# Optimization experiments

Measured on AMD Instinct MI355X. Metric: run time of the kernel, lower is better.

## Reference

```python
import jax, jax.numpy as jnp
import numpy as np

NQ = 6; DM = 128; CH = 4; SEQ = 2048; CHUNK = 16; BATCH = 128
NFP = 5 * NQ * 2   # feature params for 2 layers
NMP = 5 * NQ * 2   # mixing params for 2 layers

# ---- batched gate matrices (theta: (B,)) ----

def _rx(t):
    c = jnp.cos(t / 2).astype(jnp.complex64)
    s = (-1j * jnp.sin(t / 2)).astype(jnp.complex64)
    return jnp.stack([jnp.stack([c, s], -1), jnp.stack([s, c], -1)], -2)

def _ry(t):
    c = jnp.cos(t / 2).astype(jnp.complex64)
    s = jnp.sin(t / 2).astype(jnp.complex64)
    return jnp.stack([jnp.stack([c, -s], -1), jnp.stack([s, c], -1)], -2)

def _rz(t):
    e = jnp.exp(-1j * t.astype(jnp.complex64) / 2)
    z = jnp.zeros_like(e)
    return jnp.stack([jnp.stack([e, z], -1), jnp.stack([z, jnp.conj(e)], -1)], -2)

def _crx(t):
    B = t.shape[0]
    r = _rx(t)
    I = jnp.broadcast_to(jnp.eye(2, dtype=jnp.complex64), (B, 2, 2))
    Z = jnp.zeros((B, 2, 2), jnp.complex64)
    return jnp.concatenate([jnp.concatenate([I, Z], -1), jnp.concatenate([Z, r], -1)], -2)

# ---- batched statevector gate application; state: (B, 2, ..., 2) with axis 1+w = wire w ----

def _ap1(s, U, w):
    s = jnp.moveaxis(s, 1 + w, 1)
    sh = s.shape
    s = jnp.einsum('bij,bjr->bir', U, s.reshape(sh[0], 2, -1)).reshape(sh)
    return jnp.moveaxis(s, 1, 1 + w)

def _ap2(s, U, w0, w1):
    s = jnp.moveaxis(s, (1 + w0, 1 + w1), (1, 2))
    sh = s.shape
    s = jnp.einsum('bij,bjr->bir', U, s.reshape(sh[0], 4, -1)).reshape(sh)
    return jnp.moveaxis(s, (1, 2), (1 + w0, 1 + w1))

def _ansatz(s, p, off):
    # RX,RY,RZ on each qubit, then forward CRX ring, then backward CRX ring
    for i in range(NQ):
        s = _ap1(s, _rx(p[:, off + 3 * i]), i)
        s = _ap1(s, _ry(p[:, off + 3 * i + 1]), i)
        s = _ap1(s, _rz(p[:, off + 3 * i + 2]), i)
    off += 3 * NQ
    for i in range(NQ):
        s = _ap2(s, _crx(p[:, off]), i, (i + 1) % NQ)
        off += 1
    for i in range(NQ - 1, -1, -1):
        s = _ap2(s, _crx(p[:, off]), i, (i - 1) % NQ)
        off += 1
    return s, off

def _circuit(angles, fp, mp):
    B = angles.shape[0]
    s = jnp.zeros((B, 2 ** NQ), jnp.complex64).at[:, 0].set(1.0).reshape((B,) + (2,) * NQ)
    for i in range(NQ):                      # RY input embedding
        s = _ap1(s, _ry(angles[:, i]), i)
    off = 0
    for _ in range(2):                        # feature layers
        s, off = _ansatz(s, fp, off)
    off = 0
    for _ in range(2):                        # mixing layers
        s, off = _ansatz(s, mp, off)
    xs, ys, zs = [], [], []
    for i in range(NQ):                       # <X_i>, <Y_i>, <Z_i>
        v = jnp.moveaxis(s, 1 + i, 1).reshape(B, 2, -1)
        a, b = v[:, 0], v[:, 1]
        ab = jnp.sum(jnp.conj(a) * b, -1)
        xs.append(2 * jnp.real(ab))
        ys.append(2 * jnp.imag(ab))
        zs.append(jnp.sum(jnp.abs(a) ** 2 - jnp.abs(b) ** 2, -1))
    return jnp.stack(xs + ys + zs, 1)         # (B, 18) ordered X..Y..Z

def _ln(x, g, b, eps=1e-5):
    m = x.mean(-1, keepdims=True)
    v = ((x - m) ** 2).mean(-1, keepdims=True)
    return (x - m) / jnp.sqrt(v + eps) * g + b

def _fwd(x, conv_w, conv_b, ln1_g, ln1_b, ca1_w, ca1_b, ca2_w, ca2_b, pp_w, pp_b,
         ep_w, ep_b, op_w, op_b, ln2_g, ln2_b, sa1_w, sa1_b, sa2_w, sa2_b,
         cl1_w, cl1_b, cl2_w, cl2_b):
    B, C, S = x.shape
    h = jax.lax.conv_general_dilated(x, conv_w, (1,), [(1, 1)],
                                     dimension_numbers=('NCH', 'OIH', 'NCH')) + conv_b[None, :, None]
    h = jnp.transpose(h, (0, 2, 1))           # (B, S, D)
    h = _ln(h, ln1_g, ln1_b)
    nchunks = S // CHUNK
    h = h.reshape(B * nchunks, CHUNK, DM)
    sc = jnp.tanh(h @ ca1_w + ca1_b) @ ca2_w + ca2_b
    w = jax.nn.softmax(sc, axis=1)
    summ = jnp.sum(w * h, axis=1)             # (B*nchunks, D)
    ap = summ @ pp_w + pp_b
    fp, mp = ap[:, :NFP], ap[:, NFP:]
    ang = jnp.tanh(summ @ ep_w + ep_b) * np.pi
    q = _circuit(ang, fp, mp)                 # (B*nchunks, 18)
    cf = jax.nn.silu(_ln(q @ op_w + op_b, ln2_g, ln2_b))  # dropout = eval identity
    cf = cf.reshape(B, nchunks, DM)
    ss = jnp.tanh(cf @ sa1_w + sa1_b) @ sa2_w + sa2_b
    sw = jax.nn.softmax(ss, axis=1)
    rep = jnp.sum(sw * cf, axis=1)
    return jax.nn.silu(rep @ cl1_w + cl1_b) @ cl2_w + cl2_b

def setup_inputs() -> dict:
    key = jax.random.key(0)
    ks = jax.random.split(key, 16)
    n = lambda k, sh: (jax.random.normal(k, sh, jnp.float32) * 0.05)
    return {
        'x': jax.random.normal(ks[0], (BATCH, CH, SEQ), jnp.float32),
        'conv_w': n(ks[1], (DM, CH, 3)), 'conv_b': jnp.zeros((DM,), jnp.float32),
        'ln1_g': jnp.ones((DM,), jnp.float32), 'ln1_b': jnp.zeros((DM,), jnp.float32),
        'ca1_w': n(ks[2], (DM, DM // 4)), 'ca1_b': jnp.zeros((DM // 4,), jnp.float32),
        'ca2_w': n(ks[3], (DM // 4, 1)), 'ca2_b': jnp.zeros((1,), jnp.float32),
        'pp_w': n(ks[4], (DM, NFP + NMP)), 'pp_b': jnp.zeros((NFP + NMP,), jnp.float32),
        'ep_w': n(ks[5], (DM, NQ)), 'ep_b': jnp.zeros((NQ,), jnp.float32),
        'op_w': n(ks[6], (3 * NQ, DM)), 'op_b': jnp.zeros((DM,), jnp.float32),
        'ln2_g': jnp.ones((DM,), jnp.float32), 'ln2_b': jnp.zeros((DM,), jnp.float32),
        'sa1_w': n(ks[7], (DM, DM // 4)), 'sa1_b': jnp.zeros((DM // 4,), jnp.float32),
        'sa2_w': n(ks[8], (DM // 4, 1)), 'sa2_b': jnp.zeros((1,), jnp.float32),
        'cl1_w': n(ks[9], (DM, DM // 2)), 'cl1_b': jnp.zeros((DM // 2,), jnp.float32),
        'cl2_w': n(ks[10], (DM // 2, 2)), 'cl2_b': jnp.zeros((2,), jnp.float32),
    }

def reference(x, conv_w, conv_b, ln1_g, ln1_b, ca1_w, ca1_b, ca2_w, ca2_b, pp_w, pp_b,
              ep_w, ep_b, op_w, op_b, ln2_g, ln2_b, sa1_w, sa1_b, sa2_w, sa2_b,
              cl1_w, cl1_b, cl2_w, cl2_b):
    return _fwd(x, conv_w, conv_b, ln1_g, ln1_b, ca1_w, ca1_b, ca2_w, ca2_b, pp_w, pp_b,
                ep_w, ep_b, op_w, op_b, ln2_g, ln2_b, sa1_w, sa1_b, sa2_w, sa2_b,
                cl1_w, cl1_b, cl2_w, cl2_b)
```

## Files before the change

kernel.cpp:

```cpp
#include <hip/hip_runtime.h>
#include <math.h>


constexpr int kNQ    = 6;
constexpr int kDM    = 128;
constexpr int kCH    = 4;
constexpr int kSEQ   = 2048;
constexpr int kCHUNK = 16;
constexpr int kBATCH = 128;
constexpr int kNCH   = kSEQ / kCHUNK;
constexpr int kNP    = 120;
constexpr float kPI  = 3.14159265358979323846f;

typedef __attribute__((ext_vector_type(8))) short bf16x8;
typedef __attribute__((ext_vector_type(4))) float f32x4;

__device__ __forceinline__ float fast_tanh(float x) {
  float e = __expf(-2.f * fabsf(x));
  float r = (1.f - e) * __builtin_amdgcn_rcpf(1.f + e);
  return copysignf(r, x);
}
__device__ __forceinline__ float fast_silu(float x) {
  return x * __builtin_amdgcn_rcpf(1.f + __expf(-x));
}

template <int XM>
__device__ __forceinline__ float qp(float v) {
  constexpr int ctrl = (XM == 1) ? 0xB1 : 0x4E;
  return __int_as_float(
      __builtin_amdgcn_update_dpp(0, __float_as_int(v), ctrl, 0xF, 0xF, true));
}


template <int RB>
__device__ __forceinline__ void rx_reg(float c, float s, float* sr, float* si) {
#pragma unroll
  for (int r0 = 0; r0 < 16; ++r0) {
    if (r0 & RB) continue;
    int r1 = r0 | RB;
    float ar = sr[r0], ai = si[r0], br = sr[r1], bi = si[r1];
    sr[r0] = fmaf(c, ar,  s * bi);  si[r0] = fmaf(c, ai, -s * br);
    sr[r1] = fmaf(c, br,  s * ai);  si[r1] = fmaf(c, bi, -s * ar);
  }
}

template <int RB>
__device__ __forceinline__ void ry_reg(float c, float s, float* sr, float* si) {
#pragma unroll
  for (int r0 = 0; r0 < 16; ++r0) {
    if (r0 & RB) continue;
    int r1 = r0 | RB;
    float ar = sr[r0], ai = si[r0], br = sr[r1], bi = si[r1];
    sr[r0] = fmaf(c, ar, -s * br);  si[r0] = fmaf(c, ai, -s * bi);
    sr[r1] = fmaf(s, ar,  c * br);  si[r1] = fmaf(s, ai,  c * bi);
  }
}

template <int RB>
__device__ __forceinline__ void rz_reg(float c, float s, float* sr, float* si) {
#pragma unroll
  for (int r = 0; r < 16; ++r) {
    float sp = (r & RB) ? s : -s;
    float ar = sr[r], ai = si[r];
    sr[r] = fmaf(c, ar, -sp * ai);
    si[r] = fmaf(c, ai,  sp * ar);
  }
}

template <int XM>
__device__ __forceinline__ void rx_lane(float c, float s, float* sr, float* si) {
#pragma unroll
  for (int r = 0; r < 16; ++r) {
    float pr = qp<XM>(sr[r]), pi = qp<XM>(si[r]);
    sr[r] = fmaf(c, sr[r],  s * pi);
    si[r] = fmaf(c, si[r], -s * pr);
  }
}

template <int XM>
__device__ __forceinline__ void ry_lane(float c, float sg, float* sr, float* si) {
#pragma unroll
  for (int r = 0; r < 16; ++r) {
    float pr = qp<XM>(sr[r]), pi = qp<XM>(si[r]);
    sr[r] = fmaf(c, sr[r], sg * pr);
    si[r] = fmaf(c, si[r], sg * pi);
  }
}

__device__ __forceinline__ void rz_lane(float c, float sp, float* sr, float* si) {
#pragma unroll
  for (int r = 0; r < 16; ++r) {
    float ar = sr[r], ai = si[r];
    sr[r] = fmaf(c, ar, -sp * ai);
    si[r] = fmaf(c, ai,  sp * ar);
  }
}

template <int RB, int CB>
__device__ __forceinline__ void crx_reg_reg(float c, float s, float* sr, float* si) {
#pragma unroll
  for (int r0 = 0; r0 < 16; ++r0) {
    if ((r0 & RB) || !(r0 & CB)) continue;
    int r1 = r0 | RB;
    float ar = sr[r0], ai = si[r0], br = sr[r1], bi = si[r1];
    sr[r0] = fmaf(c, ar,  s * bi);  si[r0] = fmaf(c, ai, -s * br);
    sr[r1] = fmaf(c, br,  s * ai);  si[r1] = fmaf(c, bi, -s * ar);
  }
}

template <int XM, int CB>
__device__ __forceinline__ void crx_reg_lane(float c, float s, float* sr, float* si) {
#pragma unroll
  for (int r = 0; r < 16; ++r) {
    if (!(r & CB)) continue;
    float pr = qp<XM>(sr[r]), pi = qp<XM>(si[r]);
    sr[r] = fmaf(c, sr[r],  s * pi);
    si[r] = fmaf(c, si[r], -s * pr);
  }
}

template <int RB>
__device__ __forceinline__ void meas_reg(const float* sr, const float* si,
                                         float& tr, float& ti, float& zz) {
  tr = 0.f; ti = 0.f; zz = 0.f;
#pragma unroll
  for (int r0 = 0; r0 < 16; ++r0) {
    float n = fmaf(sr[r0], sr[r0], si[r0] * si[r0]);
    zz += (r0 & RB) ? -n : n;
    if (r0 & RB) continue;
    int r1 = r0 | RB;
    tr = fmaf(sr[r0], sr[r1], fmaf(si[r0], si[r1], tr));
    ti = fmaf(sr[r0], si[r1], fmaf(-si[r0], sr[r1], ti));
  }
  tr += qp<1>(tr); tr += qp<2>(tr);
  ti += qp<1>(ti); ti += qp<2>(ti);
  zz += qp<1>(zz); zz += qp<2>(zz);
}


__device__ __forceinline__ void circ_from_cs(const float2* __restrict__ cp,
                                             int l, int b0, int b1,
                                             float* __restrict__ res) {
  float sr[16], si[16];
#pragma unroll
  for (int r = 0; r < 16; ++r) { sr[r] = 0.f; si[r] = 0.f; }
  sr[0] = (l == 0) ? 1.f : 0.f;

  {
    float2 q0 = cp[0], q1 = cp[1], q2 = cp[2], q3 = cp[3], q4 = cp[4], q5 = cp[5];
    ry_lane<2>(q0.x, b0 ? q0.y : -q0.y, sr, si);
    ry_lane<1>(q1.x, b1 ? q1.y : -q1.y, sr, si);
    ry_reg<8>(q2.x, q2.y, sr, si);
    ry_reg<4>(q3.x, q3.y, sr, si);
    ry_reg<2>(q4.x, q4.y, sr, si);
    ry_reg<1>(q5.x, q5.y, sr, si);
  }

  for (int a = 0; a < 4; ++a) {
    const float2* pb = cp + 6 + a * 30;
    float2 t;
    t = pb[0];  rx_lane<2>(t.x, t.y, sr, si);
    t = pb[1];  ry_lane<2>(t.x, b0 ? t.y : -t.y, sr, si);
    t = pb[2];  rz_lane   (t.x, b0 ? t.y : -t.y, sr, si);
    t = pb[3];  rx_lane<1>(t.x, t.y, sr, si);
    t = pb[4];  ry_lane<1>(t.x, b1 ? t.y : -t.y, sr, si);
    t = pb[5];  rz_lane   (t.x, b1 ? t.y : -t.y, sr, si);
    t = pb[6];  rx_reg<8>(t.x, t.y, sr, si);
    t = pb[7];  ry_reg<8>(t.x, t.y, sr, si);
    t = pb[8];  rz_reg<8>(t.x, t.y, sr, si);
    t = pb[9];  rx_reg<4>(t.x, t.y, sr, si);
    t = pb[10]; ry_reg<4>(t.x, t.y, sr, si);
    t = pb[11]; rz_reg<4>(t.x, t.y, sr, si);
    t = pb[12]; rx_reg<2>(t.x, t.y, sr, si);
    t = pb[13]; ry_reg<2>(t.x, t.y, sr, si);
    t = pb[14]; rz_reg<2>(t.x, t.y, sr, si);
    t = pb[15]; rx_reg<1>(t.x, t.y, sr, si);
    t = pb[16]; ry_reg<1>(t.x, t.y, sr, si);
    t = pb[17]; rz_reg<1>(t.x, t.y, sr, si);
    t = pb[18]; { float c2 = b0 ? t.x : 1.f, s2 = b0 ? t.y : 0.f; rx_lane<1>(c2, s2, sr, si); }
    t = pb[19]; { float c2 = b1 ? t.x : 1.f, s2 = b1 ? t.y : 0.f; rx_reg<8>(c2, s2, sr, si); }
    t = pb[20]; crx_reg_reg<4, 8>(t.x, t.y, sr, si);
    t = pb[21]; crx_reg_reg<2, 4>(t.x, t.y, sr, si);
    t = pb[22]; crx_reg_reg<1, 2>(t.x, t.y, sr, si);
    t = pb[23]; crx_reg_lane<2, 1>(t.x, t.y, sr, si);
    t = pb[24]; crx_reg_reg<2, 1>(t.x, t.y, sr, si);
    t = pb[25]; crx_reg_reg<4, 2>(t.x, t.y, sr, si);
    t = pb[26]; crx_reg_reg<8, 4>(t.x, t.y, sr, si);
    t = pb[27]; crx_reg_lane<1, 8>(t.x, t.y, sr, si);
    t = pb[28]; { float c2 = b1 ? t.x : 1.f, s2 = b1 ? t.y : 0.f; rx_lane<2>(c2, s2, sr, si); }
    t = pb[29]; { float c2 = b0 ? t.x : 1.f, s2 = b0 ? t.y : 0.f; rx_reg<1>(c2, s2, sr, si); }
  }

  {
    float tr = 0.f, ti = 0.f, zz = 0.f;
#pragma unroll
    for (int r = 0; r < 16; ++r) {
      float pr = qp<2>(sr[r]), pi = qp<2>(si[r]);
      tr = fmaf(sr[r], pr, fmaf(si[r], pi, tr));
      ti = fmaf(sr[r], pi, fmaf(-si[r], pr, ti));
      zz = fmaf(sr[r], sr[r], fmaf(si[r], si[r], zz));
    }
    tr = b0 ? 0.f : tr;  ti = b0 ? 0.f : ti;  zz = b0 ? -zz : zz;
    tr += qp<1>(tr); tr += qp<2>(tr);
    ti += qp<1>(ti); ti += qp<2>(ti);
    zz += qp<1>(zz); zz += qp<2>(zz);
    res[0] = 2.f * tr; res[6] = 2.f * ti; res[12] = zz;
  }
  {
    float tr = 0.f, ti = 0.f, zz = 0.f;
#pragma unroll
    for (int r = 0; r < 16; ++r) {
      float pr = qp<1>(sr[r]), pi = qp<1>(si[r]);
      tr = fmaf(sr[r], pr, fmaf(si[r], pi, tr));
      ti = fmaf(sr[r], pi, fmaf(-si[r], pr, ti));
      zz = fmaf(sr[r], sr[r], fmaf(si[r], si[r], zz));
    }
    tr = b1 ? 0.f : tr;  ti = b1 ? 0.f : ti;  zz = b1 ? -zz : zz;
    tr += qp<1>(tr); tr += qp<2>(tr);
    ti += qp<1>(ti); ti += qp<2>(ti);
    zz += qp<1>(zz); zz += qp<2>(zz);
    res[1] = 2.f * tr; res[7] = 2.f * ti; res[13] = zz;
  }
  {
    float tr, ti, zz;
    meas_reg<8>(sr, si, tr, ti, zz); res[2] = 2.f*tr; res[8]  = 2.f*ti; res[14] = zz;
    meas_reg<4>(sr, si, tr, ti, zz); res[3] = 2.f*tr; res[9]  = 2.f*ti; res[15] = zz;
    meas_reg<2>(sr, si, tr, ti, zz); res[4] = 2.f*tr; res[10] = 2.f*ti; res[16] = zz;
    meas_reg<1>(sr, si, tr, ti, zz); res[5] = 2.f*tr; res[11] = 2.f*ti; res[17] = zz;
  }
}


__global__ __launch_bounds__(128) void k_pre8(
    const float* __restrict__ x,
    const float* __restrict__ conv_w, const float* __restrict__ conv_b,
    const float* __restrict__ ln1_g,  const float* __restrict__ ln1_b,
    const float* __restrict__ ca1_w,  const float* __restrict__ ca1_b,
    const float* __restrict__ ca2_w,  const float* __restrict__ ca2_b,
    const float* __restrict__ pp_w,   const float* __restrict__ pp_b,
    const float* __restrict__ ep_w,   const float* __restrict__ ep_b,
    float* __restrict__ outb, int emit_cs)
{
  constexpr int NC = 8;

  __shared__ __align__(16) float xs[kCH][NC * kCHUNK + 4];
  __shared__ __align__(16) float hbuf[kCHUNK][132];
  __shared__ __align__(16) float spart[2][16];
  __shared__ __align__(16) float wl[kCHUNK];
  __shared__ __align__(16) float sums[NC][kDM];
  __shared__ float mrow[kCHUNK], irow[kCHUNK];

  const int tid    = threadIdx.x;
  const int chunk0 = blockIdx.x * NC;
  const int b      = chunk0 >> 7;
  const int tloc   = (chunk0 & 127) * kCHUNK;
  const int d      = tid;
  const int lane   = tid & 63;
  const int wv     = tid >> 6;
  const int col    = (lane & 15) + 16 * wv;
  const int qd     = lane >> 4;

  float w12[12];
  {
    const float4* cw = (const float4*)(conv_w + d * 12);
    float4 a0 = cw[0], a1 = cw[1], a2 = cw[2];
    w12[0]=a0.x; w12[1]=a0.y; w12[2]=a0.z; w12[3]=a0.w;
    w12[4]=a1.x; w12[5]=a1.y; w12[6]=a1.z; w12[7]=a1.w;
    w12[8]=a2.x; w12[9]=a2.y; w12[10]=a2.z; w12[11]=a2.w;
  }
  float cb = conv_b[d];
  float g1 = ln1_g[d], b1 = ln1_b[d];
  float cb1 = ca1_b[col], cw2 = ca2_w[col], cb2 = ca2_b[0];

  bf16x8 bhi[4], blo[4];
#pragma unroll
  for (int ks = 0; ks < 4; ++ks)
#pragma unroll
    for (int jj = 0; jj < 8; ++jj) {
      float bvf = ca1_w[(ks * 32 + qd * 8 + jj) * 32 + col];
      unsigned bb = __float_as_uint(bvf);
      bhi[ks][jj] = (short)(bb >> 16);
      float lf = bvf - __uint_as_float(bb & 0xffff0000u);
      blo[ks][jj] = (short)(__float_as_uint(lf) >> 16);
    }

#pragma unroll
  for (int ch = 0; ch < kCH; ++ch) {
#pragma unroll
    for (int base = 0; base < 2; ++base) {
      int pos = base * 128 + tid;
      if (pos < NC * kCHUNK + 2) {
        int s = tloc - 1 + pos;
        float v = 0.f;
        if (s >= 0 && s < kSEQ) v = x[((size_t)b * kCH + ch) * kSEQ + s];
        xs[ch][pos] = v;
      }
    }
  }
  __syncthreads();

  for (int c = 0; c < NC; ++c) {
    float h[kCHUNK];
#pragma unroll
    for (int t = 0; t < kCHUNK; ++t) h[t] = cb;
#pragma unroll
    for (int ch = 0; ch < kCH; ++ch) {
      const float4* xp = (const float4*)&xs[ch][c * kCHUNK];
      float4 v0 = xp[0], v1 = xp[1], v2 = xp[2], v3 = xp[3], v4 = xp[4];
      float xr[18];
      xr[0]=v0.x; xr[1]=v0.y; xr[2]=v0.z; xr[3]=v0.w;
      xr[4]=v1.x; xr[5]=v1.y; xr[6]=v1.z; xr[7]=v1.w;
      xr[8]=v2.x; xr[9]=v2.y; xr[10]=v2.z; xr[11]=v2.w;
      xr[12]=v3.x; xr[13]=v3.y; xr[14]=v3.z; xr[15]=v3.w;
      xr[16]=v4.x; xr[17]=v4.y;
      float c0 = w12[ch*3+0], c1 = w12[ch*3+1], c2 = w12[ch*3+2];
#pragma unroll
      for (int t = 0; t < kCHUNK; ++t)
        h[t] = fmaf(xr[t], c0, fmaf(xr[t+1], c1, fmaf(xr[t+2], c2, h[t])));
    }
#pragma unroll
    for (int t = 0; t < kCHUNK; ++t) hbuf[t][d] = h[t];
    __syncthreads();

    {
      int row = tid >> 3, k = tid & 7;
      const float4* rp = (const float4*)&hbuf[row][k * 16];
      float s1 = 0.f, s2 = 0.f;
#pragma unroll
      for (int q = 0; q < 4; ++q) {
        float4 v = rp[q];
        s1 += v.x + v.y + v.z + v.w;
        s2 = fmaf(v.x,v.x,s2); s2 = fmaf(v.y,v.y,s2);
        s2 = fmaf(v.z,v.z,s2); s2 = fmaf(v.w,v.w,s2);
      }
#pragma unroll
      for (int o = 1; o < 8; o <<= 1) {
        s1 += __shfl_xor(s1, o, 64);
        s2 += __shfl_xor(s2, o, 64);
      }
      if (k == 0) {
        float m = s1 * (1.f / kDM);
        mrow[row] = m;
        irow[row] = rsqrtf(s2 * (1.f / kDM) - m * m + 1e-5f);
      }
    }
    __syncthreads();

#pragma unroll
    for (int t = 0; t < kCHUNK; ++t) {
      h[t] = fmaf((h[t] - mrow[t]) * irow[t], g1, b1);
      unsigned hb = __float_as_uint(h[t]);
      float lof = h[t] - __uint_as_float(hb & 0xffff0000u);
      unsigned pk = (hb >> 16) | (__float_as_uint(lof) & 0xffff0000u);
      ((unsigned*)&hbuf[t][0])[d] = pk;
    }
    __syncthreads();

    f32x4 acc = {0.f, 0.f, 0.f, 0.f};
    {
      const unsigned* hrow = (const unsigned*)&hbuf[lane & 15][0];
#pragma unroll
      for (int ks = 0; ks < 4; ++ks) {
        const uint4* ap = (const uint4*)(hrow + ks * 32 + qd * 8);
        uint4 w0 = ap[0], w1 = ap[1];
        bf16x8 ahi, alo;
        ahi[0] = (short)(w0.x & 0xffff); ahi[1] = (short)(w0.y & 0xffff);
        ahi[2] = (short)(w0.z & 0xffff); ahi[3] = (short)(w0.w & 0xffff);
        ahi[4] = (short)(w1.x & 0xffff); ahi[5] = (short)(w1.y & 0xffff);
        ahi[6] = (short)(w1.z & 0xffff); ahi[7] = (short)(w1.w & 0xffff);
        alo[0] = (short)(w0.x >> 16); alo[1] = (short)(w0.y >> 16);
        alo[2] = (short)(w0.z >> 16); alo[3] = (short)(w0.w >> 16);
        alo[4] = (short)(w1.x >> 16); alo[5] = (short)(w1.y >> 16);
        alo[6] = (short)(w1.z >> 16); alo[7] = (short)(w1.w >> 16);
        acc = __builtin_amdgcn_mfma_f32_16x16x32_bf16(ahi, bhi[ks], acc, 0, 0, 0);
        acc = __builtin_amdgcn_mfma_f32_16x16x32_bf16(ahi, blo[ks], acc, 0, 0, 0);
        acc = __builtin_amdgcn_mfma_f32_16x16x32_bf16(alo, bhi[ks], acc, 0, 0, 0);
      }
    }

    {
      float ev[4];
#pragma unroll
      for (int r = 0; r < 4; ++r)
        ev[r] = fast_tanh(acc[r] + cb1) * cw2;
#pragma unroll
      for (int o = 1; o < 16; o <<= 1)
#pragma unroll
        for (int r = 0; r < 4; ++r) ev[r] += __shfl_xor(ev[r], o, 64);
      if ((lane & 15) == 0)
        *(float4*)&spart[wv][qd * 4] = make_float4(ev[0], ev[1], ev[2], ev[3]);
    }
    __syncthreads();

    if (tid < 16) {
      float scl = spart[0][tid] + spart[1][tid] + cb2;
      float mx = scl;
#pragma unroll
      for (int o = 1; o < 16; o <<= 1) mx = fmaxf(mx, __shfl_xor(mx, o, 64));
      float e = __expf(scl - mx);
      float se = e;
#pragma unroll
      for (int o = 1; o < 16; o <<= 1) se += __shfl_xor(se, o, 64);
      wl[tid] = e * (1.f / se);
    }
    __syncthreads();

    {
      const float4* w4 = (const float4*)wl;
      float4 wa = w4[0], wb = w4[1], wc = w4[2], wd = w4[3];
      float acc2 = 0.f;
      acc2 = fmaf(wa.x, h[0],  acc2); acc2 = fmaf(wa.y, h[1],  acc2);
      acc2 = fmaf(wa.z, h[2],  acc2); acc2 = fmaf(wa.w, h[3],  acc2);
      acc2 = fmaf(wb.x, h[4],  acc2); acc2 = fmaf(wb.y, h[5],  acc2);
      acc2 = fmaf(wb.z, h[6],  acc2); acc2 = fmaf(wb.w, h[7],  acc2);
      acc2 = fmaf(wc.x, h[8],  acc2); acc2 = fmaf(wc.y, h[9],  acc2);
      acc2 = fmaf(wc.z, h[10], acc2); acc2 = fmaf(wc.w, h[11], acc2);
      acc2 = fmaf(wd.x, h[12], acc2); acc2 = fmaf(wd.y, h[13], acc2);
      acc2 = fmaf(wd.z, h[14], acc2); acc2 = fmaf(wd.w, h[15], acc2);
      sums[c][d] = acc2;
    }
  }
  __syncthreads();

  if (tid < kNP + kNQ) {
    const bool isep = (tid >= kNP);
    const int  jj   = tid - kNP;
    const float* wp = isep ? (ep_w + jj) : (pp_w + tid);
    const int  ws   = isep ? kNQ : kNP;
    const int  ws2  = ws * 2, ws3 = ws * 3, ws4 = ws * 4;
    float bias = isep ? ep_b[jj] : pp_b[tid];
    float accp[NC];
#pragma unroll
    for (int c = 0; c < NC; ++c) accp[c] = bias;
#pragma unroll 4
    for (int q4 = 0; q4 < 32; ++q4) {
      float w0 = wp[0], w1 = wp[ws], w2 = wp[ws2], w3 = wp[ws3];
      wp += ws4;
#pragma unroll
      for (int c = 0; c < NC; ++c) {
        float4 s = *(const float4*)&sums[c][q4 * 4];
        accp[c] = fmaf(s.x, w0, fmaf(s.y, w1, fmaf(s.z, w2, fmaf(s.w, w3, accp[c]))));
      }
    }
    const int slot = isep ? jj : (6 + tid);
#pragma unroll
    for (int c = 0; c < NC; ++c) {
      int chunkg = chunk0 + c;
      float ha = isep ? (0.5f * fast_tanh(accp[c]) * kPI) : (0.5f * accp[c]);
      if (emit_cs) {
        ((float2*)(outb + (size_t)chunkg * 256))[slot] =
            make_float2(__cosf(ha), __sinf(ha));
      } else {
        outb[(size_t)chunkg * 126 + slot] = ha;
      }
    }
  }
}


constexpr int kCsStride = 260;

__global__ __launch_bounds__(256) void k_circ_post(
    const float* __restrict__ csA,
    const float* __restrict__ op_w, const float* __restrict__ op_b,
    const float* __restrict__ ln2_g, const float* __restrict__ ln2_b,
    const float* __restrict__ sa1_w, const float* __restrict__ sa1_b,
    const float* __restrict__ sa2_w, const float* __restrict__ sa2_b,
    float* __restrict__ cf, float* __restrict__ sclb)
{
  __shared__ __align__(16) float lds[16 * kCsStride];
  __shared__ __align__(16) float qvs[16][19];
  __shared__ __align__(16) float cfs[2][132];
  __shared__ float part1[2][32];
  __shared__ float redA[2][2], redB[2][2];

  const int tid = threadIdx.x;

  {
    const float4* src = (const float4*)(csA + (size_t)blockIdx.x * 16 * 256);
#pragma unroll
    for (int jq = 0; jq < 4; ++jq) {
      int idx = jq * 256 + tid;
      int ic = idx >> 6, ln = idx & 63;
      *(float4*)&lds[ic * kCsStride + ln * 4] = src[idx];
    }
  }
  __syncthreads();

  if (tid < 64) {
    const int c  = tid >> 2;
    const int l  = tid & 3;
    const int b0 = (l >> 1) & 1;
    const int b1 = l & 1;
    float res[18];
    circ_from_cs((const float2*)&lds[c * kCsStride], l, b0, b1, res);
    if (l == 0) {
#pragma unroll
      for (int k = 0; k < 18; ++k) qvs[c][k] = res[k];
    }
  }

  const int d    = tid & 127;
  const int slot = tid >> 7;
  const int j    = d & 31;
  const int sub  = d >> 5;
  float ow[18];
#pragma unroll
  for (int k = 0; k < 18; ++k) ow[k] = op_w[k * kDM + d];
  float ob = op_b[d], g2 = ln2_g[d], b2 = ln2_b[d];
  float wreg[32];
  {
    const float* wp2 = sa1_w + (sub * 32) * 32 + j;
#pragma unroll
    for (int k = 0; k < 32; ++k) wreg[k] = wp2[k * 32];
  }
  float s1b = sa1_b[j], s2w = sa2_w[j], s2b = sa2_b[0];
  __syncthreads();

  for (int i = 0; i < 8; ++i) {
    const int c      = slot * 8 + i;
    const int chunkg = blockIdx.x * 16 + c;

    float qv[18];
#pragma unroll
    for (int k = 0; k < 18; ++k) qv[k] = qvs[c][k];
    float acc = ob;
#pragma unroll
    for (int k = 0; k < 18; ++k) acc = fmaf(qv[k], ow[k], acc);

    float v = acc, v2 = acc * acc;
#pragma unroll
    for (int o = 32; o; o >>= 1) { v += __shfl_xor(v, o, 64); v2 += __shfl_xor(v2, o, 64); }
    if ((d & 63) == 0) { redA[slot][d >> 6] = v; redB[slot][d >> 6] = v2; }
    __syncthreads();
    float ss1 = redA[slot][0] + redA[slot][1];
    float ss2 = redB[slot][0] + redB[slot][1];
    float m = ss1 * (1.f / kDM);
    float var = ss2 * (1.f / kDM) - m * m;
    float xn = fmaf((acc - m) * rsqrtf(var + 1e-5f), g2, b2);
    float cfv = fast_silu(xn);
    cf[(size_t)chunkg * kDM + d] = cfv;
    cfs[slot][d] = cfv;
    __syncthreads();

    float acc2 = 0.f;
#pragma unroll
    for (int q = 0; q < 8; ++q) {
      float4 hv = *(const float4*)&cfs[slot][sub * 32 + q * 4];
      acc2 = fmaf(hv.x, wreg[q*4+0], acc2);
      acc2 = fmaf(hv.y, wreg[q*4+1], acc2);
      acc2 = fmaf(hv.z, wreg[q*4+2], acc2);
      acc2 = fmaf(hv.w, wreg[q*4+3], acc2);
    }
    acc2 += __shfl_xor(acc2, 32, 64);
    if (sub == 2) part1[slot][j] = acc2;
    __syncthreads();
    if (d < 32) {
      float hv = fast_tanh(acc2 + part1[slot][j] + s1b) * s2w;
#pragma unroll
      for (int o = 16; o; o >>= 1) hv += __shfl_xor(hv, o, 64);
      if (j == 0) sclb[chunkg] = hv + s2b;
    }
  }
}


__global__ __launch_bounds__(64) void k_circ_cs(const float* __restrict__ csA,
                                                float* __restrict__ qv_g)
{
  __shared__ __align__(16) float lds[16 * kCsStride];

  const int lane  = threadIdx.x;
  const int c     = lane >> 2;
  const int l     = lane & 3;
  const int chunk = blockIdx.x * 16 + c;
  const int b0 = (l >> 1) & 1;
  const int b1 = l & 1;

  {
    const float4* src = (const float4*)(csA + (size_t)blockIdx.x * 16 * 256);
#pragma unroll
    for (int i = 0; i < 16; ++i) {
      float4 v = src[i * 64 + lane];
      *(float4*)&lds[i * kCsStride + lane * 4] = v;
    }
  }
  __syncthreads();

  float res[18];
  circ_from_cs((const float2*)&lds[c * kCsStride], l, b0, b1, res);

  if (l == 0) {
    float* qo = qv_g + (size_t)chunk * 18;
#pragma unroll
    for (int k = 0; k < 18; ++k) qo[k] = res[k];
  }
}


__global__ __launch_bounds__(64) void k_circ(const float* __restrict__ csb_g,
                                             float* __restrict__ qv_g)
{
  const int lane  = threadIdx.x;
  const int c     = lane >> 2;
  const int l     = lane & 3;
  const int chunk = blockIdx.x * 16 + c;
  const float* cp = csb_g + (size_t)chunk * 126;
  const int b0 = (l >> 1) & 1;
  const int b1 = l & 1;

  float sr[16], si[16];
#pragma unroll
  for (int r = 0; r < 16; ++r) { sr[r] = 0.f; si[r] = 0.f; }
  sr[0] = (l == 0) ? 1.f : 0.f;

  {
    float gc[6], gs[6];
#pragma unroll
    for (int g = 0; g < 6; ++g) { float th = cp[g]; gc[g] = __cosf(th); gs[g] = __sinf(th); }
    ry_lane<2>(gc[0], b0 ? gs[0] : -gs[0], sr, si);
    ry_lane<1>(gc[1], b1 ? gs[1] : -gs[1], sr, si);
    ry_reg<8>(gc[2], gs[2], sr, si);
    ry_reg<4>(gc[3], gs[3], sr, si);
    ry_reg<2>(gc[4], gs[4], sr, si);
    ry_reg<1>(gc[5], gs[5], sr, si);
  }

  for (int a = 0; a < 4; ++a) {
    const float* pb = cp + 6 + a * 30;
    float gc[30], gs[30];
#pragma unroll
    for (int g = 0; g < 30; ++g) { float th = pb[g]; gc[g] = __cosf(th); gs[g] = __sinf(th); }
    rx_lane<2>(gc[0], gs[0], sr, si);
    ry_lane<2>(gc[1], b0 ? gs[1] : -gs[1], sr, si);
    rz_lane   (gc[2], b0 ? gs[2] : -gs[2], sr, si);
    rx_lane<1>(gc[3], gs[3], sr, si);
    ry_lane<1>(gc[4], b1 ? gs[4] : -gs[4], sr, si);
    rz_lane   (gc[5], b1 ? gs[5] : -gs[5], sr, si);
    rx_reg<8>(gc[6],  gs[6],  sr, si);  ry_reg<8>(gc[7],  gs[7],  sr, si);  rz_reg<8>(gc[8],  gs[8],  sr, si);
    rx_reg<4>(gc[9],  gs[9],  sr, si);  ry_reg<4>(gc[10], gs[10], sr, si);  rz_reg<4>(gc[11], gs[11], sr, si);
    rx_reg<2>(gc[12], gs[12], sr, si);  ry_reg<2>(gc[13], gs[13], sr, si);  rz_reg<2>(gc[14], gs[14], sr, si);
    rx_reg<1>(gc[15], gs[15], sr, si);  ry_reg<1>(gc[16], gs[16], sr, si);  rz_reg<1>(gc[17], gs[17], sr, si);
    { float c2 = b0 ? gc[18] : 1.f, s2 = b0 ? gs[18] : 0.f; rx_lane<1>(c2, s2, sr, si); }
    { float c2 = b1 ? gc[19] : 1.f, s2 = b1 ? gs[19] : 0.f; rx_reg<8>(c2, s2, sr, si); }
    crx_reg_reg<4, 8>(gc[20], gs[20], sr, si);
    crx_reg_reg<2, 4>(gc[21], gs[21], sr, si);
    crx_reg_reg<1, 2>(gc[22], gs[22], sr, si);
    crx_reg_lane<2, 1>(gc[23], gs[23], sr, si);
    crx_reg_reg<2, 1>(gc[24], gs[24], sr, si);
    crx_reg_reg<4, 2>(gc[25], gs[25], sr, si);
    crx_reg_reg<8, 4>(gc[26], gs[26], sr, si);
    crx_reg_lane<1, 8>(gc[27], gs[27], sr, si);
    { float c2 = b1 ? gc[28] : 1.f, s2 = b1 ? gs[28] : 0.f; rx_lane<2>(c2, s2, sr, si); }
    { float c2 = b0 ? gc[29] : 1.f, s2 = b0 ? gs[29] : 0.f; rx_reg<1>(c2, s2, sr, si); }
  }

  float res[18];
  {
    float tr = 0.f, ti = 0.f, zz = 0.f;
#pragma unroll
    for (int r = 0; r < 16; ++r) {
      float pr = qp<2>(sr[r]), pi = qp<2>(si[r]);
      tr = fmaf(sr[r], pr, fmaf(si[r], pi, tr));
      ti = fmaf(sr[r], pi, fmaf(-si[r], pr, ti));
      zz = fmaf(sr[r], sr[r], fmaf(si[r], si[r], zz));
    }
    tr = b0 ? 0.f : tr;  ti = b0 ? 0.f : ti;  zz = b0 ? -zz : zz;
    tr += qp<1>(tr); tr += qp<2>(tr);
    ti += qp<1>(ti); ti += qp<2>(ti);
    zz += qp<1>(zz); zz += qp<2>(zz);
    res[0] = 2.f * tr; res[6] = 2.f * ti; res[12] = zz;
  }
  {
    float tr = 0.f, ti = 0.f, zz = 0.f;
#pragma unroll
    for (int r = 0; r < 16; ++r) {
      float pr = qp<1>(sr[r]), pi = qp<1>(si[r]);
      tr = fmaf(sr[r], pr, fmaf(si[r], pi, tr));
      ti = fmaf(sr[r], pi, fmaf(-si[r], pr, ti));
      zz = fmaf(sr[r], sr[r], fmaf(si[r], si[r], zz));
    }
    tr = b1 ? 0.f : tr;  ti = b1 ? 0.f : ti;  zz = b1 ? -zz : zz;
    tr += qp<1>(tr); tr += qp<2>(tr);
    ti += qp<1>(ti); ti += qp<2>(ti);
    zz += qp<1>(zz); zz += qp<2>(zz);
    res[1] = 2.f * tr; res[7] = 2.f * ti; res[13] = zz;
  }
  {
    float tr, ti, zz;
    meas_reg<8>(sr, si, tr, ti, zz); res[2] = 2.f*tr; res[8]  = 2.f*ti; res[14] = zz;
    meas_reg<4>(sr, si, tr, ti, zz); res[3] = 2.f*tr; res[9]  = 2.f*ti; res[15] = zz;
    meas_reg<2>(sr, si, tr, ti, zz); res[4] = 2.f*tr; res[10] = 2.f*ti; res[16] = zz;
    meas_reg<1>(sr, si, tr, ti, zz); res[5] = 2.f*tr; res[11] = 2.f*ti; res[17] = zz;
  }
  if (l == 0) {
    float* qo = qv_g + (size_t)chunk * 18;
#pragma unroll
    for (int k = 0; k < 18; ++k) qo[k] = res[k];
  }
}


__global__ __launch_bounds__(128) void k_post(
    const float* __restrict__ qv_g,
    const float* __restrict__ op_w, const float* __restrict__ op_b,
    const float* __restrict__ ln2_g, const float* __restrict__ ln2_b,
    const float* __restrict__ sa1_w, const float* __restrict__ sa1_b,
    const float* __restrict__ sa2_w, const float* __restrict__ sa2_b,
    float* __restrict__ cf, float* __restrict__ sclb)
{
  __shared__ float cfs[132];
  __shared__ float part1[32];
  __shared__ float red[4];

  const int chunk = blockIdx.x, tid = threadIdx.x, d = tid;
  const int j = tid & 31, sub = tid >> 5;

  float qv[18];
  {
    const float* qpp = qv_g + (size_t)chunk * 18;
#pragma unroll
    for (int k = 0; k < 18; ++k) qv[k] = qpp[k];
  }
  float acc = op_b[d];
#pragma unroll
  for (int k = 0; k < 18; ++k) acc = fmaf(qv[k], op_w[k * kDM + d], acc);

  float v = acc, v2 = acc * acc;
#pragma unroll
  for (int o = 32; o; o >>= 1) { v += __shfl_xor(v, o, 64); v2 += __shfl_xor(v2, o, 64); }
  if ((tid & 63) == 0) { red[tid >> 6] = v; red[2 + (tid >> 6)] = v2; }
  __syncthreads();
  float s1 = red[0] + red[1], s2 = red[2] + red[3];
  float m = s1 * (1.f / kDM);
  float var = s2 * (1.f / kDM) - m * m;
  float xn = fmaf((acc - m) * rsqrtf(var + 1e-5f), ln2_g[d], ln2_b[d]);
  float cfv = fast_silu(xn);
  cf[(size_t)chunk * kDM + d] = cfv;
  cfs[d] = cfv;
  __syncthreads();

  float acc2 = 0.f;
  {
    const float* wp2 = sa1_w + (sub * 32) * 32 + j;
#pragma unroll
    for (int q = 0; q < 8; ++q) {
      float4 hv = *(const float4*)&cfs[sub * 32 + q * 4];
      acc2 = fmaf(hv.x, wp2[(q*4+0)*32], acc2);
      acc2 = fmaf(hv.y, wp2[(q*4+1)*32], acc2);
      acc2 = fmaf(hv.z, wp2[(q*4+2)*32], acc2);
      acc2 = fmaf(hv.w, wp2[(q*4+3)*32], acc2);
    }
  }
  acc2 += __shfl_xor(acc2, 32, 64);
  if (sub == 2) part1[j] = acc2;
  __syncthreads();
  if (tid < 32) {
    float hv = fast_tanh(acc2 + part1[j] + sa1_b[j]) * sa2_w[j];
#pragma unroll
    for (int o = 16; o; o >>= 1) hv += __shfl_xor(hv, o, 64);
    if (j == 0) sclb[chunk] = hv + sa2_b[0];
  }
}


__global__ __launch_bounds__(512) void k_pool_cf(
    const float* __restrict__ cf, const float* __restrict__ scl,
    const float* __restrict__ cl1_w, const float* __restrict__ cl1_b,
    const float* __restrict__ cl2_w, const float* __restrict__ cl2_b,
    float* __restrict__ out)
{
  __shared__ float wl[kNCH];
  __shared__ float rep4[4][kDM];
  __shared__ float ulp[8][64];
  __shared__ float ul[64];
  __shared__ float red2[16];
  int b = blockIdx.x, tid = threadIdx.x;
  int idx = tid & 127, wid = tid >> 6;
  float s = scl[b*kNCH + idx];
  float mx = s;
#pragma unroll
  for (int o = 32; o; o >>= 1) mx = fmaxf(mx, __shfl_xor(mx,o,64));
  if ((tid & 63) == 0) red2[wid] = mx;
  __syncthreads();
  mx = fmaxf(red2[0], red2[1]);
  float e = __expf(s - mx);
  float se = e;
#pragma unroll
  for (int o = 32; o; o >>= 1) se += __shfl_xor(se,o,64);
  if ((tid & 63) == 0) red2[8+wid] = se;
  if (tid < kNCH) wl[tid] = e;
  __syncthreads();
  float inv = 1.f/(red2[8]+red2[9]);
  {
    int dd = tid & 127, qq = tid >> 7;
    const float* cfb = cf + (size_t)b*kNCH*kDM + (size_t)qq*32*kDM;
    const float* wlq = wl + qq*32;
    float a0=0,a1=0,a2=0,a3=0;
// ... 385 lines not shown
```

Before: 192.0 us.

## Fuse per-qubit RX/RY/RZ rotations into single precomputed 2x2 unitaries

Adds a cooperative pre-pass where all 256 threads compose each qubit's RX·RY·RZ triple (and the input RY embedding for the first layer) into one general 2x2 complex unitary and store it in shared memory. The circuit simulation then applies one generic gate per qubit instead of three or four separate rotations, which cuts per-thread gate work in the serial 64-thread circuit phase. In exchange it adds an extra shared buffer, another barrier, and denser complex arithmetic per gate application.

```diff
diff --git a/kernel.cpp b/kernel.cpp
--- a/kernel.cpp
+++ b/kernel.cpp
@@ -135,6 +135,38 @@
   tr += qp<1>(tr); tr += qp<2>(tr);
   ti += qp<1>(ti); ti += qp<2>(ti);
   zz += qp<1>(zz); zz += qp<2>(zz);
+}
+
+
+template <int RB>
+__device__ __forceinline__ void gen_reg(const float4 u0, const float4 u1,
+                                        float* sr, float* si) {
+#pragma unroll
+  for (int r0 = 0; r0 < 16; ++r0) {
+    if (r0 & RB) continue;
+    int r1 = r0 | RB;
+    float p0r = sr[r0], p0i = si[r0], p1r = sr[r1], p1i = si[r1];
+    sr[r0] = fmaf(u0.x, p0r, fmaf(-u0.y, p0i, fmaf(u0.z, p1r, -u0.w * p1i)));
+    si[r0] = fmaf(u0.x, p0i, fmaf( u0.y, p0r, fmaf(u0.z, p1i,  u0.w * p1r)));
+    sr[r1] = fmaf(u1.x, p0r, fmaf(-u1.y, p0i, fmaf(u1.z, p1r, -u1.w * p1i)));
+    si[r1] = fmaf(u1.x, p0i, fmaf( u1.y, p0r, fmaf(u1.z, p1i,  u1.w * p1r)));
+  }
+}
+
+template <int XM>
+__device__ __forceinline__ void gen_lane(const float4 u0, const float4 u1,
+                                         int bsel, float* sr, float* si) {
+  float m0r = bsel ? u1.z : u0.x;
+  float m0i = bsel ? u1.w : u0.y;
+  float m1r = bsel ? u1.x : u0.z;
+  float m1i = bsel ? u1.y : u0.w;
+#pragma unroll
+  for (int r = 0; r < 16; ++r) {
+    float pr = qp<XM>(sr[r]), pi = qp<XM>(si[r]);
+    float xr = sr[r], xi = si[r];
+    sr[r] = fmaf(m0r, xr, fmaf(-m0i, xi, fmaf(m1r, pr, -m1i * pi)));
+    si[r] = fmaf(m0r, xi, fmaf( m0i, xr, fmaf(m1r, pi,  m1i * pr)));
+  }
 }
 
 
@@ -231,6 +263,80 @@
 }
 
 
+__device__ __forceinline__ void circ_fused(const float2* __restrict__ cp,
+                                           const float* __restrict__ fp,
+                                           int l, int b0, int b1,
+                                           float* __restrict__ res) {
+  float sr[16], si[16];
+#pragma unroll
+  for (int r = 0; r < 16; ++r) { sr[r] = 0.f; si[r] = 0.f; }
+  sr[0] = (l == 0) ? 1.f : 0.f;
+
+  for (int a = 0; a < 4; ++a) {
+    const float4* fg = (const float4*)(fp + a * 48);
+    gen_lane<2>(fg[0],  fg[1],  b0, sr, si);
+    gen_lane<1>(fg[2],  fg[3],  b1, sr, si);
+    gen_reg<8> (fg[4],  fg[5],  sr, si);
+    gen_reg<4> (fg[6],  fg[7],  sr, si);
+    gen_reg<2> (fg[8],  fg[9],  sr, si);
+    gen_reg<1> (fg[10], fg[11], sr, si);
+
+    const float2* pb = cp + 6 + a * 30;
+    float2 t;
+    t = pb[18]; { float c2 = b0 ? t.x : 1.f, s2 = b0 ? t.y : 0.f; rx_lane<1>(c2, s2, sr, si); }
+    t = pb[19]; { float c2 = b1 ? t.x : 1.f, s2 = b1 ? t.y : 0.f; rx_reg<8>(c2, s2, sr, si); }
+    t = pb[20]; crx_reg_reg<4, 8>(t.x, t.y, sr, si);
+    t = pb[21]; crx_reg_reg<2, 4>(t.x, t.y, sr, si);
+    t = pb[22]; crx_reg_reg<1, 2>(t.x, t.y, sr, si);
+    t = pb[23]; crx_reg_lane<2, 1>(t.x, t.y, sr, si);
+    t = pb[24]; crx_reg_reg<2, 1>(t.x, t.y, sr, si);
+    t = pb[25]; crx_reg_reg<4, 2>(t.x, t.y, sr, si);
+    t = pb[26]; crx_reg_reg<8, 4>(t.x, t.y, sr, si);
+    t = pb[27]; crx_reg_lane<1, 8>(t.x, t.y, sr, si);
+    t = pb[28]; { float c2 = b1 ? t.x : 1.f, s2 = b1 ? t.y : 0.f; rx_lane<2>(c2, s2, sr, si); }
+    t = pb[29]; { float c2 = b0 ? t.x : 1.f, s2 = b0 ? t.y : 0.f; rx_reg<1>(c2, s2, sr, si); }
+  }
+
+  {
+    float tr = 0.f, ti = 0.f, zz = 0.f;
+#pragma unroll
+    for (int r = 0; r < 16; ++r) {
+      float pr = qp<2>(sr[r]), pi = qp<2>(si[r]);
+      tr = fmaf(sr[r], pr, fmaf(si[r], pi, tr));
+      ti = fmaf(sr[r], pi, fmaf(-si[r], pr, ti));
+      zz = fmaf(sr[r], sr[r], fmaf(si[r], si[r], zz));
+    }
+    tr = b0 ? 0.f : tr;  ti = b0 ? 0.f : ti;  zz = b0 ? -zz : zz;
+    tr += qp<1>(tr); tr += qp<2>(tr);
+    ti += qp<1>(ti); ti += qp<2>(ti);
+    zz += qp<1>(zz); zz += qp<2>(zz);
+    res[0] = 2.f * tr; res[6] = 2.f * ti; res[12] = zz;
+  }
+  {
+    float tr = 0.f, ti = 0.f, zz = 0.f;
+#pragma unroll
+    for (int r = 0; r < 16; ++r) {
+      float pr = qp<1>(sr[r]), pi = qp<1>(si[r]);
+      tr = fmaf(sr[r], pr, fmaf(si[r], pi, tr));
+      ti = fmaf(sr[r], pi, fmaf(-si[r], pr, ti));
+      zz = fmaf(sr[r], sr[r], fmaf(si[r], si[r], zz));
+    }
+    tr = b1 ? 0.f : tr;  ti = b1 ? 0.f : ti;  zz = b1 ? -zz : zz;
+    tr += qp<1>(tr); tr += qp<2>(tr);
+    ti += qp<1>(ti); ti += qp<2>(ti);
+    zz += qp<1>(zz); zz += qp<2>(zz);
+    res[1] = 2.f * tr; res[7] = 2.f * ti; res[13] = zz;
+  }
+  {
+    float tr, ti, zz;
+    meas_reg<8>(sr, si, tr, ti, zz); res[2] = 2.f*tr; res[8]  = 2.f*ti; res[14] = zz;
+    meas_reg<4>(sr, si, tr, ti, zz); res[3] = 2.f*tr; res[9]  = 2.f*ti; res[15] = zz;
+    meas_reg<2>(sr, si, tr, ti, zz); res[4] = 2.f*tr; res[10] = 2.f*ti; res[16] = zz;
+    meas_reg<1>(sr, si, tr, ti, zz); res[5] = 2.f*tr; res[11] = 2.f*ti; res[17] = zz;
+  }
+}
+
+
 __global__ __launch_bounds__(128) void k_pre8(
     const float* __restrict__ x,
     const float* __restrict__ conv_w, const float* __restrict__ conv_b,
@@ -459,6 +565,7 @@
 
 
 constexpr int kCsStride = 260;
+constexpr int kFuStride = 196;
 
 __global__ __launch_bounds__(256) void k_circ_post(
     const float* __restrict__ csA,
@@ -469,6 +576,7 @@
     float* __restrict__ cf, float* __restrict__ sclb)
 {
   __shared__ __align__(16) float lds[16 * kCsStride];
+  __shared__ __align__(16) float fused[16 * kFuStride];
   __shared__ __align__(16) float qvs[16][19];
   __shared__ __align__(16) float cfs[2][132];
   __shared__ float part1[2][32];
@@ -484,6 +592,41 @@
       int ic = idx >> 6, ln = idx & 63;
       *(float4*)&lds[ic * kCsStride + ln * 4] = src[idx];
     }
+  }
+  __syncthreads();
+
+  for (int m = tid; m < 16 * 24; m += 256) {
+    const int chunk = m / 24;
+    const int g     = m % 24;
+    const int a     = g / 6, q = g - a * 6;
+    const float2* cp = (const float2*)&lds[chunk * kCsStride];
+    float2 t1 = cp[6 + 30 * a + 3 * q + 0];
+    float2 t2 = cp[6 + 30 * a + 3 * q + 1];
+    float2 t3 = cp[6 + 30 * a + 3 * q + 2];
+    float A00r =  t2.x * t1.x, A00i =  t2.y * t1.y;
+    float A01r = -t2.y * t1.x, A01i = -t2.x * t1.y;
+    float A10r =  t2.y * t1.x, A10i = -t2.x * t1.y;
+    float A11r =  t2.x * t1.x, A11i = -t2.y * t1.y;
+    if (a == 0) {
+      float2 t0 = cp[q];
+      float B00r = fmaf(A00r, t0.x,  A01r * t0.y), B00i = fmaf(A00i, t0.x,  A01i * t0.y);
+      float B01r = fmaf(A01r, t0.x, -A00r * t0.y), B01i = fmaf(A01i, t0.x, -A00i * t0.y);
+      float B10r = fmaf(A10r, t0.x,  A11r * t0.y), B10i = fmaf(A10i, t0.x,  A11i * t0.y);
+      float B11r = fmaf(A11r, t0.x, -A10r * t0.y), B11i = fmaf(A11i, t0.x, -A10i * t0.y);
+      A00r = B00r; A00i = B00i; A01r = B01r; A01i = B01i;
+      A10r = B10r; A10i = B10i; A11r = B11r; A11i = B11i;
+    }
+    float4 u0 = make_float4(fmaf(t3.x, A00r,  t3.y * A00i),
+                            fmaf(t3.x, A00i, -t3.y * A00r),
+                            fmaf(t3.x, A01r,  t3.y * A01i),
+                            fmaf(t3.x, A01i, -t3.y * A01r));
+    float4 u1 = make_float4(fmaf(t3.x, A10r, -t3.y * A10i),
+                            fmaf(t3.x, A10i,  t3.y * A10r),
+                            fmaf(t3.x, A11r, -t3.y * A11i),
+                            fmaf(t3.x, A11i,  t3.y * A11r));
+    float4* fb = (float4*)&fused[chunk * kFuStride + g * 8];
+    fb[0] = u0;
+    fb[1] = u1;
   }
   __syncthreads();
 
@@ -493,7 +636,8 @@
     const int b0 = (l >> 1) & 1;
     const int b1 = l & 1;
     float res[18];
-    circ_from_cs((const float2*)&lds[c * kCsStride], l, b0, b1, res);
+    circ_fused((const float2*)&lds[c * kCsStride], &fused[c * kFuStride],
+               l, b0, b1, res);
     if (l == 0) {
 #pragma unroll
       for (int k = 0; k < 18; ++k) qvs[c][k] = res[k];
```

New measurement: 193.5 us. No clear change (+0.7%).
